# Optimization experiments

Hardware: AMD Instinct MI355X
Metric: run time of the kernel (lower is better)

Reference implementation:

```python
import jax, jax.numpy as jnp
import numpy as np

B, L, D, H, N = 8, 2048, 128, 4, 2
DK = D // H          # 32
DFF = 2 * D          # 256 (dff = d * 2 in source)


def _init_proj(key, shape):
    # matches torch init: uniform in [-s, s], s = sqrt(6/(fan_in+fan_out)) of last two dims
    s = np.sqrt(6.0 / (shape[-1] + shape[-2]))
    return jax.random.uniform(key, shape, jnp.float32, -s, s)


def setup_inputs() -> dict:
    key = jax.random.key(0)
    ks = jax.random.split(key, 8)
    x = jax.random.normal(ks[0], (B, L, D), jnp.float32)
    mask = jnp.ones((B, L), jnp.float32)
    Wq = _init_proj(ks[1], (N, H, D, DK))
    Wk = _init_proj(ks[2], (N, H, D, DK))
    Wv = _init_proj(ks[3], (N, H, D, DK))
    Wo = _init_proj(ks[4], (N, H * DK, D))
    W1 = _init_proj(ks[5], (N, D, DFF))
    b1 = jnp.zeros((N, 1, 1, DFF), jnp.float32)
    W2 = _init_proj(ks[6], (N, DFF, D))
    b2 = jnp.zeros((N, 1, 1, D), jnp.float32)
    return {"x": x, "mask": mask, "Wq": Wq, "Wk": Wk, "Wv": Wv,
            "Wo": Wo, "W1": W1, "b1": b1, "W2": W2, "b2": b2}


def reference(x, mask, Wq, Wk, Wv, Wo, W1, b1, W2, b2):
    # Eval-mode forward (no attention dropout-mask trick, no FFN dropout).
    neg = jnp.finfo(x.dtype).min
    m2 = mask[:, :, None] * mask[:, None, :]              # [B, L, L]
    add_mask = (1.0 - m2)[:, None, :, :] * neg            # [B, 1, L, L]
    bsz, max_len, _ = x.shape
    for i in range(N):  # small fixed layer loop
        q = jnp.einsum('bld,hde->bhle', x, Wq[i])         # [B,H,L,DK]
        k = jnp.einsum('bld,hde->bhle', x, Wk[i])
        v = jnp.einsum('bld,hde->bhle', x, Wv[i])
        A = jnp.einsum('bhqe,bhke->bhqk', q, k) + add_mask  # note: no 1/sqrt(dk), as in source
        A = jax.nn.softmax(A, axis=-1)                    # [B,H,L,L]
        o = jnp.einsum('bhqk,bhke->bqhe', A, v)           # [B,L,H,DK]
        o = o.reshape(bsz, max_len, H * DK) @ Wo[i]       # [B,L,D]
        x = (o + x) / 2
        f = jax.nn.gelu(x @ W1[i] + b1[i], approximate=False)  # torch F.gelu is exact erf
        f = f @ W2[i] + b2[i]
        x = (f + x) / 2
    return x
```

## Files before the change

### kernel.cpp

```cpp
#include <hip/hip_runtime.h>
#include <math.h>

#define BB 8
#define LL 2048
#define DD 128
#define HH 4
#define DKK 32
#define DFFF 256

#define NEGMIN (-3.402823466e38f)
#define LOG2E 1.44269504088896f

typedef _Float16 f16;
typedef _Float16 f16x4 __attribute__((ext_vector_type(4)));
typedef _Float16 f16x8 __attribute__((ext_vector_type(8)));
typedef __fp16 h16x2 __attribute__((ext_vector_type(2)));
typedef float f32x4 __attribute__((ext_vector_type(4)));

union PKU { h16x2 h2[2]; f16x4 v; };

__global__ __launch_bounds__(256) void xcvt_kernel(const float* __restrict__ x,
                                                   f16* __restrict__ xh) {
  const int i = (blockIdx.x * 256 + threadIdx.x) * 8;
  float4 v0 = *(const float4*)(x + i);
  float4 v1 = *(const float4*)(x + i + 4);
  f16x8 h;
  h[0] = (f16)v0.x; h[1] = (f16)v0.y; h[2] = (f16)v0.z; h[3] = (f16)v0.w;
  h[4] = (f16)v1.x; h[5] = (f16)v1.y; h[6] = (f16)v1.z; h[7] = (f16)v1.w;
  *(f16x8*)(xh + i) = h;
}

__global__ __launch_bounds__(256) void maskchk_kernel(
    const float* __restrict__ mask, int* __restrict__ flags) {
  __shared__ int wok[4];
  const int b = blockIdx.x, t = threadIdx.x;
  bool ok = true;
  for (int i = t; i < LL; i += 256) ok &= (mask[b * LL + i] == 1.f);
  const bool all_ok = __all(ok);
  if ((t & 63) == 0) wok[t >> 6] = all_ok ? 1 : 0;
  __syncthreads();
  if (t == 0) flags[b] = wok[0] & wok[1] & wok[2] & wok[3];
}

__global__ __launch_bounds__(256) void wconv_kernel(
    const float* __restrict__ Wq, const float* __restrict__ Wk,
    const float* __restrict__ Wv, const float* __restrict__ Wo,
    const float* __restrict__ W1, const float* __restrict__ W2,
    f16* __restrict__ wt) {
  const int idx = blockIdx.x * 256 + threadIdx.x;
  const int i = idx >> 17;
  const int r = idx & 131071;
  float val;
  if (r < 49152) {
    const int sel = r / 16384;
    const int rr = r & 16383;
    const int n = rr >> 7, k = rr & 127;
    const float* W = (sel == 0) ? Wq : (sel == 1) ? Wk : Wv;
    val = W[((size_t)(i * 4 + (n >> 5)) * 128 + k) * 32 + (n & 31)];
  } else if (r < 65536) {
    const int r2 = r - 49152;
    const int n = r2 >> 7, k = r2 & 127;
    val = Wo[i * 16384 + k * 128 + n];
  } else if (r < 98304) {
    const int r2 = r - 65536;
    const int n = r2 >> 7, k = r2 & 127;
    val = W1[i * 32768 + k * 256 + n];
  } else {
    const int r2 = r - 98304;
    const int n = r2 >> 8, k = r2 & 255;
    val = W2[i * 32768 + k * 128 + n];
  }
  wt[idx] = (f16)val;
}

__global__ __launch_bounds__(256) void qkv_kernel(
    const f16* __restrict__ xh, const f16* __restrict__ wqkvT,
    f16* __restrict__ qh, f16* __restrict__ kh, f16* __restrict__ vth) {
  const int t = threadIdx.x;
  const int wave = t >> 6, lane = t & 63;
  const int g = lane >> 4, c = lane & 15;
  const int r0g = blockIdx.x * 64 + wave * 16;
  const int b4 = (r0g >> 11) * 4;
  const int l0 = r0g & 2047;

  f16x8 a[4];
#pragma unroll
  for (int kt = 0; kt < 4; ++kt)
    a[kt] = *(const f16x8*)(xh + (size_t)(r0g + c) * 128 + kt * 32 + g * 8);

#pragma unroll
  for (int sel = 0; sel < 2; ++sel) {
    const f16* wT = wqkvT + sel * 16384;
    f16* out = (sel == 0) ? qh : kh;
#pragma unroll
    for (int nt = 0; nt < 8; ++nt) {
      f32x4 acc = {0.f, 0.f, 0.f, 0.f};
#pragma unroll
      for (int kt = 0; kt < 4; ++kt) {
        f16x8 bfrag = *(const f16x8*)(wT + (nt * 16 + c) * 128 + kt * 32 + g * 8);
        acc = __builtin_amdgcn_mfma_f32_16x16x32_f16(a[kt], bfrag, acc, 0, 0, 0);
      }
      const int h = nt >> 1, e = (nt & 1) * 16 + c;
#pragma unroll
      for (int r = 0; r < 4; ++r)
        out[((size_t)(b4 + h) * LL + l0 + 4 * g + r) * DKK + e] = (f16)acc[r];
    }
  }
  {
    const f16* wT = wqkvT + 2 * 16384;
#pragma unroll
    for (int nt = 0; nt < 8; ++nt) {
      f32x4 acc = {0.f, 0.f, 0.f, 0.f};
#pragma unroll
      for (int kt = 0; kt < 4; ++kt) {
        f16x8 afrag = *(const f16x8*)(wT + (nt * 16 + c) * 128 + kt * 32 + g * 8);
        acc = __builtin_amdgcn_mfma_f32_16x16x32_f16(afrag, a[kt], acc, 0, 0, 0);
      }
#pragma unroll
      for (int r = 0; r < 4; ++r) {
        const int eg = nt * 16 + 4 * g + r;
        vth[((size_t)(b4 + (eg >> 5)) * DKK + (eg & 31)) * LL + l0 + c] =
            (f16)acc[r];
      }
    }
  }
}

__global__ __launch_bounds__(256, 4) void attn_kernel(
    const f16* __restrict__ qh, const f16* __restrict__ kh,
    const f16* __restrict__ vth, const float* __restrict__ mask,
    const int* __restrict__ bflags, f16* __restrict__ o) {
  __shared__ f16 Vt[4][2][32][72];
  const int t = threadIdx.x;
  const int wave = t >> 6, lane = t & 63;
  const int g = lane >> 4, c = lane & 15;

  const int flat = blockIdx.x;
  const int xcd = flat & 7, slot = flat >> 3;
  const int bh = xcd * 4 + (slot >> 4);
  const int qb = slot & 15;
  const int b = bh >> 2;
  const int qw = qb * 128 + wave * 32;
  const bool nomask_b = (bflags[b] != 0);

  f16x8 qfrag[2];
  float mqv[2] = {1.f, 1.f};
#pragma unroll
  for (int qt = 0; qt < 2; ++qt)
    qfrag[qt] =
        *(const f16x8*)(qh + ((size_t)bh * LL + qw + qt * 16 + c) * DKK + g * 8);
  if (!nomask_b) {
#pragma unroll
    for (int qt = 0; qt < 2; ++qt) mqv[qt] = mask[b * LL + qw + qt * 16 + c];
  }

  f32x4 o4[2][2];
  float m[2], l[2];
#pragma unroll
  for (int qt = 0; qt < 2; ++qt) {
    m[qt] = -3.0e38f; l[qt] = 0.f;
#pragma unroll
    for (int dt = 0; dt < 2; ++dt)
#pragma unroll
      for (int r = 0; r < 4; ++r) o4[qt][dt][r] = 0.f;
  }

  const f16* kp = kh + (size_t)bh * LL * DKK + (size_t)c * DKK + g * 8;
  const int vd = lane >> 3, vseg = lane & 7;
  const f16* vp = vth + (size_t)bh * DKK * LL + (size_t)vd * LL + vseg * 8;

#define LOADK(DST, KT)                                       \
  {                                                          \
    const f16* _p = kp + (size_t)(KT) * 64 * DKK;            \
    DST[0] = *(const f16x8*)(_p);                            \
    DST[1] = *(const f16x8*)(_p + 16 * DKK);                 \
    DST[2] = *(const f16x8*)(_p + 32 * DKK);                 \
    DST[3] = *(const f16x8*)(_p + 48 * DKK);                 \
  }
#define LOADVREG(DST, KT)                                    \
  {                                                          \
    const f16* _p = vp + (KT) * 64;                          \
    DST[0] = *(const f16x8*)(_p);                            \
    DST[1] = *(const f16x8*)(_p + 8 * LL);                   \
    DST[2] = *(const f16x8*)(_p + 16 * LL);                  \
    DST[3] = *(const f16x8*)(_p + 24 * LL);                  \
  }
#define COMMITV(SRC, BUF)                                    \
  {                                                          \
    *(f16x8*)&Vt[wave][BUF][vd][vseg * 8] = SRC[0];          \
    *(f16x8*)&Vt[wave][BUF][vd + 8][vseg * 8] = SRC[1];      \
    *(f16x8*)&Vt[wave][BUF][vd + 16][vseg * 8] = SRC[2];     \
    *(f16x8*)&Vt[wave][BUF][vd + 24][vseg * 8] = SRC[3];     \
  }

  f16x8 kbA[4], kbB[4], vr[4];

  LOADVREG(vr, 0);
  LOADK(kbA, 0);
  COMMITV(vr, 0);

  for (int kt = 0; kt < 32; ++kt) {
    const int cur = kt & 1;
    if (kt < 31) {
      LOADK(kbB, kt + 1);
      LOADVREG(vr, kt + 1);
    }

    f32x4 st[2][4];
    __builtin_amdgcn_s_setprio(1);
#pragma unroll
    for (int qt = 0; qt < 2; ++qt)
#pragma unroll
      for (int nt = 0; nt < 4; ++nt) {
        f32x4 z = {0.f, 0.f, 0.f, 0.f};
        st[qt][nt] =
            __builtin_amdgcn_mfma_f32_16x16x32_f16(kbA[nt], qfrag[qt], z, 0, 0, 0);
      }
    __builtin_amdgcn_s_setprio(0);

    if (!nomask_b) {
      const int k0 = kt * 64;
#pragma unroll
      for (int qt = 0; qt < 2; ++qt) {
        const float mq = mqv[qt];
#pragma unroll
        for (int nt = 0; nt < 4; ++nt) {
          float4 mk4 = *(const float4*)(mask + b * LL + k0 + nt * 16 + 4 * g);
          st[qt][nt][0] += (1.f - mq * mk4.x) * NEGMIN;
          st[qt][nt][1] += (1.f - mq * mk4.y) * NEGMIN;
          st[qt][nt][2] += (1.f - mq * mk4.z) * NEGMIN;
          st[qt][nt][3] += (1.f - mq * mk4.w) * NEGMIN;
        }
      }
    }

    f16x4 va[2][4];
#pragma unroll
    for (int dt = 0; dt < 2; ++dt)
#pragma unroll
      for (int nt = 0; nt < 4; ++nt)
        va[dt][nt] = *(const f16x4*)&Vt[wave][cur][dt * 16 + c][nt * 16 + 4 * g];

#pragma unroll
    for (int qt = 0; qt < 2; ++qt) {
      float vmax = fmaxf(fmaxf(st[qt][0][0], st[qt][0][1]),
                         fmaxf(st[qt][0][2], st[qt][0][3]));
#pragma unroll
      for (int nt = 1; nt < 4; ++nt)
        vmax = fmaxf(vmax, fmaxf(fmaxf(st[qt][nt][0], st[qt][nt][1]),
                                 fmaxf(st[qt][nt][2], st[qt][nt][3])));
      vmax = fmaxf(vmax, __shfl_xor(vmax, 16));
      vmax = fmaxf(vmax, __shfl_xor(vmax, 32));

      if (!__all(vmax - m[qt] <= 8.f)) {
        const float mn = fmaxf(m[qt], vmax);
        const float sc = __builtin_exp2f((m[qt] - mn) * LOG2E);
        l[qt] *= sc;
#pragma unroll
        for (int dt = 0; dt < 2; ++dt)
#pragma unroll
          for (int r = 0; r < 4; ++r) o4[qt][dt][r] *= sc;
        m[qt] = mn;
      }
      const float mn2 = m[qt] * LOG2E;

      float p[4][4];
      float psum = 0.f;
#pragma unroll
      for (int nt = 0; nt < 4; ++nt) {
#pragma unroll
        for (int r = 0; r < 4; ++r) {
          p[nt][r] = __builtin_exp2f(fmaf(st[qt][nt][r], LOG2E, -mn2));
          psum += p[nt][r];
        }
      }
      l[qt] += psum;

      __builtin_amdgcn_s_setprio(1);
#pragma unroll
      for (int nt = 0; nt < 4; ++nt) {
        PKU pk;
        pk.h2[0] = __builtin_amdgcn_cvt_pkrtz(p[nt][0], p[nt][1]);
        pk.h2[1] = __builtin_amdgcn_cvt_pkrtz(p[nt][2], p[nt][3]);
        o4[qt][0] = __builtin_amdgcn_mfma_f32_16x16x16f16(va[0][nt], pk.v,
                                                          o4[qt][0], 0, 0, 0);
        o4[qt][1] = __builtin_amdgcn_mfma_f32_16x16x16f16(va[1][nt], pk.v,
                                                          o4[qt][1], 0, 0, 0);
      }
      __builtin_amdgcn_s_setprio(0);
    }

    if (kt < 31) {
      COMMITV(vr, 1 - cur);
#pragma unroll
      for (int i = 0; i < 4; ++i) kbA[i] = kbB[i];
    }
  }
#undef LOADK
#undef LOADVREG
#undef COMMITV

  const int h = bh & 3;
#pragma unroll
  for (int qt = 0; qt < 2; ++qt) {
    float lt = l[qt];
    lt += __shfl_xor(lt, 16);
    lt += __shfl_xor(lt, 32);
    const float rdiv = 1.f / lt;
    f16* orow = o + ((size_t)b * LL + qw + qt * 16 + c) * DD + h * DKK;
#pragma unroll
    for (int dt = 0; dt < 2; ++dt) {
      f16x4 res;
      res[0] = (f16)(o4[qt][dt][0] * rdiv);
      res[1] = (f16)(o4[qt][dt][1] * rdiv);
      res[2] = (f16)(o4[qt][dt][2] * rdiv);
      res[3] = (f16)(o4[qt][dt][3] * rdiv);
      *(f16x4*)(orow + dt * 16 + g * 4) = res;
    }
  }
}

__global__ __launch_bounds__(256) void mlp_kernel(
    const f16* __restrict__ o, const float* __restrict__ x,
    const f16* __restrict__ WoT, const f16* __restrict__ W1T,
    const f16* __restrict__ W2T, const float* __restrict__ b1,
    const float* __restrict__ b2, float* __restrict__ xout,
    const f16* __restrict__ wqkvT_next,
    f16* __restrict__ qh, f16* __restrict__ kh, f16* __restrict__ vth) {
  __shared__ f16 Xm[64][136];
  __shared__ f16 Fs[64][264];
  const int t = threadIdx.x;
  const int wave = t >> 6, lane = t & 63;
  const int g = lane >> 4, c = lane & 15;
  const int mrow = wave * 16;
  const long r0 = (long)blockIdx.x * 64;

  f16x8 a1[4];
#pragma unroll
  for (int kt = 0; kt < 4; ++kt)
    a1[kt] = *(const f16x8*)(o + (r0 + mrow + c) * 128 + kt * 32 + g * 8);

  f32x4 xmreg[8];
#pragma unroll
  for (int nt = 0; nt < 8; ++nt) {
    f32x4 acc = {0.f, 0.f, 0.f, 0.f};
#pragma unroll
    for (int kt = 0; kt < 4; ++kt) {
      f16x8 bfrag = *(const f16x8*)(WoT + (nt * 16 + c) * 128 + kt * 32 + g * 8);
      acc = __builtin_amdgcn_mfma_f32_16x16x32_f16(a1[kt], bfrag, acc, 0, 0, 0);
    }
#pragma unroll
    for (int r = 0; r < 4; ++r) {
      const float xv = x[(r0 + mrow + 4 * g + r) * 128 + nt * 16 + c];
      acc[r] = (acc[r] + xv) * 0.5f;
      Xm[mrow + 4 * g + r][nt * 16 + c] = (f16)acc[r];
    }
    xmreg[nt] = acc;
  }

  f16x8 a2[4];
#pragma unroll
  for (int kt = 0; kt < 4; ++kt)
    a2[kt] = *(const f16x8*)&Xm[mrow + c][kt * 32 + g * 8];
#pragma unroll
  for (int nt = 0; nt < 16; ++nt) {
    f32x4 acc = {0.f, 0.f, 0.f, 0.f};
#pragma unroll
    for (int kt = 0; kt < 4; ++kt) {
      f16x8 bfrag = *(const f16x8*)(W1T + (nt * 16 + c) * 128 + kt * 32 + g * 8);
      acc = __builtin_amdgcn_mfma_f32_16x16x32_f16(a2[kt], bfrag, acc, 0, 0, 0);
    }
    const float bj = b1[nt * 16 + c];
#pragma unroll
    for (int r = 0; r < 4; ++r) {
      const float val = acc[r] + bj;
      Fs[mrow + 4 * g + r][nt * 16 + c] =
          (f16)(0.5f * val * (1.f + erff(val * 0.70710678118654752f)));
    }
  }

  f16x8 a3[8];
#pragma unroll
  for (int kt = 0; kt < 8; ++kt)
    a3[kt] = *(const f16x8*)&Fs[mrow + c][kt * 32 + g * 8];
#pragma unroll
  for (int nt = 0; nt < 8; ++nt) {
    f32x4 acc = {0.f, 0.f, 0.f, 0.f};
#pragma unroll
    for (int kt = 0; kt < 8; ++kt) {
      f16x8 bfrag = *(const f16x8*)(W2T + (nt * 16 + c) * 256 + kt * 32 + g * 8);
      acc = __builtin_amdgcn_mfma_f32_16x16x32_f16(a3[kt], bfrag, acc, 0, 0, 0);
    }
    const float bj = b2[nt * 16 + c];
#pragma unroll
    for (int r = 0; r < 4; ++r) {
      const float val = (acc[r] + bj + xmreg[nt][r]) * 0.5f;
      xout[(r0 + mrow + 4 * g + r) * 128 + nt * 16 + c] = val;
      Xm[mrow + 4 * g + r][nt * 16 + c] = (f16)val;
    }
  }

  if (wqkvT_next) {
    const int r0g = (int)r0 + mrow;
    const int b4 = (r0g >> 11) * 4;
    const int l0 = r0g & 2047;
    f16x8 a[4];
#pragma unroll
    for (int kt = 0; kt < 4; ++kt)
      a[kt] = *(const f16x8*)&Xm[mrow + c][kt * 32 + g * 8];

#pragma unroll
    for (int sel = 0; sel < 2; ++sel) {
      const f16* wT = wqkvT_next + sel * 16384;
      f16* out = (sel == 0) ? qh : kh;
#pragma unroll
      for (int nt = 0; nt < 8; ++nt) {
        f32x4 acc = {0.f, 0.f, 0.f, 0.f};
#pragma unroll
        for (int kt = 0; kt < 4; ++kt) {
          f16x8 bfrag =
              *(const f16x8*)(wT + (nt * 16 + c) * 128 + kt * 32 + g * 8);
          acc = __builtin_amdgcn_mfma_f32_16x16x32_f16(a[kt], bfrag, acc, 0, 0, 0);
        }
        const int h = nt >> 1, e = (nt & 1) * 16 + c;
#pragma unroll
        for (int r = 0; r < 4; ++r)
          out[((size_t)(b4 + h) * LL + l0 + 4 * g + r) * DKK + e] = (f16)acc[r];
      }
    }
    {
      const f16* wT = wqkvT_next + 2 * 16384;
#pragma unroll
      for (int nt = 0; nt < 8; ++nt) {
        f32x4 acc = {0.f, 0.f, 0.f, 0.f};
#pragma unroll
        for (int kt = 0; kt < 4; ++kt) {
          f16x8 afrag =
              *(const f16x8*)(wT + (nt * 16 + c) * 128 + kt * 32 + g * 8);
          acc = __builtin_amdgcn_mfma_f32_16x16x32_f16(afrag, a[kt], acc, 0, 0, 0);
        }
#pragma unroll
        for (int r = 0; r < 4; ++r) {
          const int eg = nt * 16 + 4 * g + r;
          vth[((size_t)(b4 + (eg >> 5)) * DKK + (eg & 31)) * LL + l0 + c] =
              (f16)acc[r];
        }
      }
    }
  }
}

extern "C" void kernel_launch(void* const* d_in, const int* in_sizes, int n_in,
                              void* d_out, int out_size, void* d_ws,
                              size_t ws_size, hipStream_t stream) {
  const float* x    = (const float*)d_in[0];
  const float* mask = (const float*)d_in[1];
  const float* Wq   = (const float*)d_in[2];
  const float* Wk   = (const float*)d_in[3];
  const float* Wv   = (const float*)d_in[4];
  const float* Wo   = (const float*)d_in[5];
  const float* W1   = (const float*)d_in[6];
  const float* b1   = (const float*)d_in[7];
  const float* W2   = (const float*)d_in[8];
  const float* b2   = (const float*)d_in[9];

  const size_t SZ = (size_t)BB * LL * DD;
  char* p = (char*)d_ws;
  f16* qh   = (f16*)p;  p += SZ * sizeof(f16);
  f16* kh   = (f16*)p;  p += SZ * sizeof(f16);
  f16* vth  = (f16*)p;  p += SZ * sizeof(f16);
  f16* ob   = (f16*)p;  p += SZ * sizeof(f16);
  f16* xh0  = (f16*)p;  p += SZ * sizeof(f16);
  f16* wt   = (f16*)p;  p += (size_t)262144 * sizeof(f16);
  int* bflags = (int*)p; p += 256;
  float* xA = (float*)p;

  wconv_kernel<<<1024, 256, 0, stream>>>(Wq, Wk, Wv, Wo, W1, W2, wt);
  xcvt_kernel<<<SZ / 8 / 256, 256, 0, stream>>>(x, xh0);
  maskchk_kernel<<<BB, 256, 0, stream>>>(mask, bflags);

  for (int i = 0; i < 2; ++i) {
    const float* xin = (i == 0) ? x : xA;
    float* xout = (i == 1) ? (float*)d_out : xA;
    const f16* qkvT_i = wt + (size_t)i * 131072;
    const f16* WoT_i  = wt + (size_t)i * 131072 + 49152;
    const f16* W1T_i  = wt + (size_t)i * 131072 + 65536;
    const f16* W2T_i  = wt + (size_t)i * 131072 + 98304;
    const float* b1_i = b1 + (long)i * DFFF;
    const float* b2_i = b2 + (long)i * DD;
    const f16* qkvT_next = (i == 0) ? (wt + 131072) : nullptr;

    if (i == 0)
      qkv_kernel<<<(BB * LL) / 64, 256, 0, stream>>>(xh0, qkvT_i, qh, kh, vth);
    attn_kernel<<<512, 256, 0, stream>>>(qh, kh, vth, mask, bflags, ob);
    mlp_kernel<<<(BB * LL) / 64, 256, 0, stream>>>(ob, xin, WoT_i, W1T_i, W2T_i,
                                                   b1_i, b2_i, xout,
                                                   qkvT_next, qh, kh, vth);
  }
}
```

Before: 210.5 us.

## Split output columns across wave pairs in QKV and MLP kernels

Each block now handles 32 rows instead of 64, with two waves per 16-row group, each computing half of the output columns in the QKV, Wo, W1, W2 and next-layer QKV projections. Grid size doubles to 512 blocks, giving more parallelism across CUs and shorter per-wave serial MFMA chains. The cost is block-level __syncthreads between stages, because waves now read shared-memory tiles written by their partner wave, and each block re-reads the same weights for half as many rows.

```diff
diff --git a/kernel.cpp b/kernel.cpp
--- a/kernel.cpp
+++ b/kernel.cpp
@@ -79,7 +79,8 @@
   const int t = threadIdx.x;
   const int wave = t >> 6, lane = t & 63;
   const int g = lane >> 4, c = lane & 15;
-  const int r0g = blockIdx.x * 64 + wave * 16;
+  const int rgrp = wave >> 1, half = wave & 1;
+  const int r0g = blockIdx.x * 32 + rgrp * 16;
   const int b4 = (r0g >> 11) * 4;
   const int l0 = r0g & 2047;
 
@@ -88,10 +89,9 @@
   for (int kt = 0; kt < 4; ++kt)
     a[kt] = *(const f16x8*)(xh + (size_t)(r0g + c) * 128 + kt * 32 + g * 8);
 
-#pragma unroll
-  for (int sel = 0; sel < 2; ++sel) {
-    const f16* wT = wqkvT + sel * 16384;
-    f16* out = (sel == 0) ? qh : kh;
+  {
+    const f16* wT = wqkvT + half * 16384;
+    f16* out = (half == 0) ? qh : kh;
 #pragma unroll
     for (int nt = 0; nt < 8; ++nt) {
       f32x4 acc = {0.f, 0.f, 0.f, 0.f};
@@ -109,16 +109,17 @@
   {
     const f16* wT = wqkvT + 2 * 16384;
 #pragma unroll
-    for (int nt = 0; nt < 8; ++nt) {
+    for (int nt = 0; nt < 4; ++nt) {
+      const int ntg = half * 4 + nt;
       f32x4 acc = {0.f, 0.f, 0.f, 0.f};
 #pragma unroll
       for (int kt = 0; kt < 4; ++kt) {
-        f16x8 afrag = *(const f16x8*)(wT + (nt * 16 + c) * 128 + kt * 32 + g * 8);
+        f16x8 afrag = *(const f16x8*)(wT + (ntg * 16 + c) * 128 + kt * 32 + g * 8);
         acc = __builtin_amdgcn_mfma_f32_16x16x32_f16(afrag, a[kt], acc, 0, 0, 0);
       }
 #pragma unroll
       for (int r = 0; r < 4; ++r) {
-        const int eg = nt * 16 + 4 * g + r;
+        const int eg = ntg * 16 + 4 * g + r;
         vth[((size_t)(b4 + (eg >> 5)) * DKK + (eg & 31)) * LL + l0 + c] =
             (f16)acc[r];
       }
@@ -327,80 +328,87 @@
     const float* __restrict__ b2, float* __restrict__ xout,
     const f16* __restrict__ wqkvT_next,
     f16* __restrict__ qh, f16* __restrict__ kh, f16* __restrict__ vth) {
-  __shared__ f16 Xm[64][136];
-  __shared__ f16 Fs[64][264];
+  __shared__ f16 Xm[32][136];
+  __shared__ f16 Fs[32][264];
   const int t = threadIdx.x;
   const int wave = t >> 6, lane = t & 63;
   const int g = lane >> 4, c = lane & 15;
-  const int mrow = wave * 16;
-  const long r0 = (long)blockIdx.x * 64;
+  const int rgrp = wave >> 1, half = wave & 1;
+  const int mrow = rgrp * 16;
+  const long r0 = (long)blockIdx.x * 32;
 
   f16x8 a1[4];
 #pragma unroll
   for (int kt = 0; kt < 4; ++kt)
     a1[kt] = *(const f16x8*)(o + (r0 + mrow + c) * 128 + kt * 32 + g * 8);
 
-  f32x4 xmreg[8];
-#pragma unroll
-  for (int nt = 0; nt < 8; ++nt) {
+  f32x4 xmreg[4];
+#pragma unroll
+  for (int nt = 0; nt < 4; ++nt) {
+    const int ntg = half * 4 + nt;
     f32x4 acc = {0.f, 0.f, 0.f, 0.f};
 #pragma unroll
     for (int kt = 0; kt < 4; ++kt) {
-      f16x8 bfrag = *(const f16x8*)(WoT + (nt * 16 + c) * 128 + kt * 32 + g * 8);
+      f16x8 bfrag = *(const f16x8*)(WoT + (ntg * 16 + c) * 128 + kt * 32 + g * 8);
       acc = __builtin_amdgcn_mfma_f32_16x16x32_f16(a1[kt], bfrag, acc, 0, 0, 0);
     }
 #pragma unroll
     for (int r = 0; r < 4; ++r) {
-      const float xv = x[(r0 + mrow + 4 * g + r) * 128 + nt * 16 + c];
+      const float xv = x[(r0 + mrow + 4 * g + r) * 128 + ntg * 16 + c];
       acc[r] = (acc[r] + xv) * 0.5f;
-      Xm[mrow + 4 * g + r][nt * 16 + c] = (f16)acc[r];
+      Xm[mrow + 4 * g + r][ntg * 16 + c] = (f16)acc[r];
     }
     xmreg[nt] = acc;
   }
+  __syncthreads();
 
   f16x8 a2[4];
 #pragma unroll
   for (int kt = 0; kt < 4; ++kt)
     a2[kt] = *(const f16x8*)&Xm[mrow + c][kt * 32 + g * 8];
 #pragma unroll
-  for (int nt = 0; nt < 16; ++nt) {
+  for (int nt = 0; nt < 8; ++nt) {
+    const int ntg = half * 8 + nt;
     f32x4 acc = {0.f, 0.f, 0.f, 0.f};
 #pragma unroll
     for (int kt = 0; kt < 4; ++kt) {
-      f16x8 bfrag = *(const f16x8*)(W1T + (nt * 16 + c) * 128 + kt * 32 + g * 8);
+      f16x8 bfrag = *(const f16x8*)(W1T + (ntg * 16 + c) * 128 + kt * 32 + g * 8);
       acc = __builtin_amdgcn_mfma_f32_16x16x32_f16(a2[kt], bfrag, acc, 0, 0, 0);
     }
-    const float bj = b1[nt * 16 + c];
+    const float bj = b1[ntg * 16 + c];
 #pragma unroll
     for (int r = 0; r < 4; ++r) {
       const float val = acc[r] + bj;
-      Fs[mrow + 4 * g + r][nt * 16 + c] =
+      Fs[mrow + 4 * g + r][ntg * 16 + c] =
           (f16)(0.5f * val * (1.f + erff(val * 0.70710678118654752f)));
     }
   }
+  __syncthreads();
 
   f16x8 a3[8];
 #pragma unroll
   for (int kt = 0; kt < 8; ++kt)
     a3[kt] = *(const f16x8*)&Fs[mrow + c][kt * 32 + g * 8];
 #pragma unroll
-  for (int nt = 0; nt < 8; ++nt) {
+  for (int nt = 0; nt < 4; ++nt) {
+    const int ntg = half * 4 + nt;
     f32x4 acc = {0.f, 0.f, 0.f, 0.f};
 #pragma unroll
     for (int kt = 0; kt < 8; ++kt) {
-      f16x8 bfrag = *(const f16x8*)(W2T + (nt * 16 + c) * 256 + kt * 32 + g * 8);
+      f16x8 bfrag = *(const f16x8*)(W2T + (ntg * 16 + c) * 256 + kt * 32 + g * 8);
       acc = __builtin_amdgcn_mfma_f32_16x16x32_f16(a3[kt], bfrag, acc, 0, 0, 0);
     }
-    const float bj = b2[nt * 16 + c];
+    const float bj = b2[ntg * 16 + c];
 #pragma unroll
     for (int r = 0; r < 4; ++r) {
       const float val = (acc[r] + bj + xmreg[nt][r]) * 0.5f;
-      xout[(r0 + mrow + 4 * g + r) * 128 + nt * 16 + c] = val;
-      Xm[mrow + 4 * g + r][nt * 16 + c] = (f16)val;
+      xout[(r0 + mrow + 4 * g + r) * 128 + ntg * 16 + c] = val;
+      Xm[mrow + 4 * g + r][ntg * 16 + c] = (f16)val;
     }
   }
 
   if (wqkvT_next) {
+    __syncthreads();
     const int r0g = (int)r0 + mrow;
     const int b4 = (r0g >> 11) * 4;
     const int l0 = r0g & 2047;
@@ -409,10 +417,9 @@
     for (int kt = 0; kt < 4; ++kt)
       a[kt] = *(const f16x8*)&Xm[mrow + c][kt * 32 + g * 8];
 
-#pragma unroll
-    for (int sel = 0; sel < 2; ++sel) {
-      const f16* wT = wqkvT_next + sel * 16384;
-      f16* out = (sel == 0) ? qh : kh;
+    {
+      const f16* wT = wqkvT_next + half * 16384;
+      f16* out = (half == 0) ? qh : kh;
 #pragma unroll
       for (int nt = 0; nt < 8; ++nt) {
         f32x4 acc = {0.f, 0.f, 0.f, 0.f};
@@ -431,17 +438,18 @@
     {
       const f16* wT = wqkvT_next + 2 * 16384;
 #pragma unroll
-      for (int nt = 0; nt < 8; ++nt) {
+      for (int nt = 0; nt < 4; ++nt) {
+        const int ntg = half * 4 + nt;
         f32x4 acc = {0.f, 0.f, 0.f, 0.f};
 #pragma unroll
         for (int kt = 0; kt < 4; ++kt) {
           f16x8 afrag =
-              *(const f16x8*)(wT + (nt * 16 + c) * 128 + kt * 32 + g * 8);
+              *(const f16x8*)(wT + (ntg * 16 + c) * 128 + kt * 32 + g * 8);
           acc = __builtin_amdgcn_mfma_f32_16x16x32_f16(afrag, a[kt], acc, 0, 0, 0);
         }
 #pragma unroll
         for (int r = 0; r < 4; ++r) {
-          const int eg = nt * 16 + 4 * g + r;
+          const int eg = ntg * 16 + 4 * g + r;
           vth[((size_t)(b4 + (eg >> 5)) * DKK + (eg & 31)) * LL + l0 + c] =
               (f16)acc[r];
         }
@@ -491,9 +499,9 @@
     const f16* qkvT_next = (i == 0) ? (wt + 131072) : nullptr;
 
     if (i == 0)
-      qkv_kernel<<<(BB * LL) / 64, 256, 0, stream>>>(xh0, qkvT_i, qh, kh, vth);
+      qkv_kernel<<<(BB * LL) / 32, 256, 0, stream>>>(xh0, qkvT_i, qh, kh, vth);
     attn_kernel<<<512, 256, 0, stream>>>(qh, kh, vth, mask, bflags, ob);
-    mlp_kernel<<<(BB * LL) / 64, 256, 0, stream>>>(ob, xin, WoT_i, W1T_i, W2T_i,
+    mlp_kernel<<<(BB * LL) / 32, 256, 0, stream>>>(ob, xin, WoT_i, W1T_i, W2T_i,
                                                    b1_i, b2_i, xout,
                                                    qkvT_next, qh, kh, vth);
   }
```

After: 208.8 us. No clear change (-0.8%).
